# Optimization experiments

Measured on AMD Instinct MI355X. Metric: run time of the kernel, lower is better.

Reference implementation:

```python
import jax, jax.numpy as jnp
import numpy as np

NEG_INF = -1e10


def setup_inputs() -> dict:
    key = jax.random.key(0)
    ks = jax.random.split(key, 9)
    B, S, H, E = 64, 4096, 512, 512
    hidden = jax.random.normal(ks[0], (B, H), dtype=jnp.float32)
    encoder_outputs = jax.random.normal(ks[1], (B, S, E), dtype=jnp.float32)
    mask = jax.random.randint(ks[2], (B, S), 0, 2, dtype=jnp.int32)
    s = 1.0 / np.sqrt(H)
    Wq = jax.random.uniform(ks[3], (H, H), jnp.float32, -s, s)
    bq = jax.random.uniform(ks[4], (H,), jnp.float32, -s, s)
    se = 1.0 / np.sqrt(E)
    Wk = jax.random.uniform(ks[5], (E, H), jnp.float32, -se, se)
    bk = jax.random.uniform(ks[6], (H,), jnp.float32, -se, se)
    Wv = jax.random.uniform(ks[7], (H, 1), jnp.float32, -s, s)
    bv = jax.random.uniform(ks[8], (1,), jnp.float32, -s, s)
    return {"hidden": hidden, "encoder_outputs": encoder_outputs, "mask": mask,
            "Wq": Wq, "bq": bq, "Wk": Wk, "bk": bk, "Wv": Wv, "bv": bv}


def reference(hidden, encoder_outputs, mask, Wq, bq, Wk, bk, Wv, bv):
    # query projection: (B, H) -> broadcast over src_len
    q = hidden @ Wq + bq                       # (B, H)
    k = jnp.einsum('bse,eh->bsh', encoder_outputs, Wk) + bk  # (B, S, H)
    energy = jnp.tanh(q[:, None, :] + k)       # (B, S, H)
    scores = jnp.einsum('bsh,h->bs', energy, Wv[:, 0]) + bv[0]  # (B, S)
    scores = jnp.where(mask == 0, NEG_INF, scores)
    attn = jax.nn.softmax(scores, axis=1)      # (B, S)
    context = jnp.einsum('bs,bse->be', attn, encoder_outputs)   # (B, E)
    return context, attn
```

## Files before the change

### kernel.cpp

```cpp
#include <hip/hip_runtime.h>
#include <hip/hip_bf16.h>

#define B_ 64
#define S_ 4096
#define H_ 512
#define E_ 512
#define NEG_INF_ -1e10f

typedef __attribute__((ext_vector_type(8))) short short8;
typedef __attribute__((ext_vector_type(16))) float f32x16;

static __device__ __forceinline__ unsigned short f2bf(float f) {
    union { float f; unsigned u; } v; v.f = f;
    unsigned x = v.u;
    x += 0x7FFFu + ((x >> 16) & 1u);
    return (unsigned short)(x >> 16);
}

static __device__ __forceinline__ unsigned pk2(float lo, float hi) {
    float2 f; f.x = lo; f.y = hi;
    union { __hip_bfloat162 h; unsigned u; } c;
    c.h = __float22bfloat162_rn(f);
    return c.u;
}

static __device__ __forceinline__ void gload_lds16(const void* g, void* l) {
    __builtin_amdgcn_global_load_lds(
        (const __attribute__((address_space(1))) void*)g,
        (__attribute__((address_space(3))) void*)l, 16, 0, 0);
}

#define VMCNT6 do { asm volatile("s_waitcnt vmcnt(6)" ::: "memory"); __builtin_amdgcn_sched_barrier(0); } while (0)
#define VMCNT0 do { asm volatile("s_waitcnt vmcnt(0)" ::: "memory"); __builtin_amdgcn_sched_barrier(0); } while (0)
#define LGKM0  do { asm volatile("s_waitcnt lgkmcnt(0)" ::: "memory"); __builtin_amdgcn_sched_barrier(0); } while (0)

__global__ void prep_wkt(const float* __restrict__ wk, unsigned short* __restrict__ wkt) {
    int idx = blockIdx.x * 256 + threadIdx.x;
    int h = idx >> 9, e = idx & 511;
    wkt[idx] = f2bf(wk[e * H_ + h]);
}

__global__ void prep_qb(const float* __restrict__ hidden, const float* __restrict__ wq,
                        const float* __restrict__ bq, const float* __restrict__ bk,
                        float* __restrict__ qb) {
    __shared__ float hid[H_];
    int b = blockIdx.x, t = threadIdx.x;
    hid[t]       = hidden[b * H_ + t];
    hid[t + 256] = hidden[b * H_ + t + 256];
    __syncthreads();
    for (int hh = t; hh < H_; hh += 256) {
        float s = 0.f;
        for (int e = 0; e < H_; ++e) s += hid[e] * wq[e * H_ + hh];
        qb[b * H_ + hh] = s + bq[hh] + bk[hh];
    }
}

__global__ __launch_bounds__(256, 4) void scores_kernel(
    const float* __restrict__ enc, const unsigned short* __restrict__ wkt,
    const float* __restrict__ qb, const float* __restrict__ wv,
    float* __restrict__ part)
{
    __shared__ char lds[40960];

    int id = blockIdx.x;
    int xcd = id & 7, qq = id >> 3;
    int logical = xcd * 1024 + qq;
    int b  = logical >> 7;
    int r  = logical & 127;
    int st = r >> 2, nt = r & 3;
    int s0 = st * 128;

    const int tid  = threadIdx.x;
    const int lane = tid & 63;
    const int wave = tid >> 6;
    const int wr   = wave >> 1;
    const int wc   = wave & 1;
    const int l31  = lane & 31;
    const int g    = lane >> 5;

    const float* encb = enc + ((size_t)b * S_ + s0) * E_;

    const int arow   = tid & 127;
    const int aksl0  = (tid >> 7) * 2;
    const float* aptr = encb + (size_t)arow * 512 + aksl0 * 8;
    const int asrow  = arow & 31;
    const int aslb   = (arow >> 5) * 4 + aksl0;
    char* const awb0 = (char*)0 + asrow * 256 + (((aslb + 0 + asrow) & 15) << 4);
    char* const awb1 = (char*)0 + asrow * 256 + (((aslb + 1 + asrow) & 15) << 4);

    auto loadA = [&](int kc, float4 (&st_)[4]) {
        const float* p = aptr + kc * 32;
        st_[0] = *(const float4*)(p);
        st_[1] = *(const float4*)(p + 4);
        st_[2] = *(const float4*)(p + 8);
        st_[3] = *(const float4*)(p + 12);
    };
    auto writeA = [&](char* buf, const float4 (&st_)[4]) {
        union { short8 s; unsigned u[4]; } u0, u1;
        u0.u[0] = pk2(st_[0].x, st_[0].y); u0.u[1] = pk2(st_[0].z, st_[0].w);
        u0.u[2] = pk2(st_[1].x, st_[1].y); u0.u[3] = pk2(st_[1].z, st_[1].w);
        u1.u[0] = pk2(st_[2].x, st_[2].y); u1.u[1] = pk2(st_[2].z, st_[2].w);
        u1.u[2] = pk2(st_[3].x, st_[3].y); u1.u[3] = pk2(st_[3].z, st_[3].w);
        *(short8*)(buf + (size_t)awb0) = u0.s;
        *(short8*)(buf + (size_t)awb1) = u1.s;
    };
    auto stageB = [&](int kc, char* buf) {
#pragma unroll
        for (int p = 0; p < 2; ++p) {
            int gi0 = p * 256 + wave * 64;
            char* db = buf + gi0 * 16;
            int gi = gi0 + lane;
            int sn = gi >> 4, ss = gi & 15;
            int sl = ss ^ (sn & 15);
            int n  = (sl >> 2) * 32 + sn;
            const unsigned short* gp = wkt + (size_t)(nt * 128 + n) * 512 + kc * 32 + (sl & 3) * 8;
            gload_lds16(gp, db);
        }
    };

    f32x16 acc[2][2];
#pragma unroll
    for (int mr = 0; mr < 2; ++mr)
#pragma unroll
        for (int nf = 0; nf < 2; ++nf)
#pragma unroll
            for (int e = 0; e < 16; ++e) acc[mr][nf][e] = 0.f;

    float4 ra[4], rb[4];

    stageB(0, lds + 16384);          loadA(0, ra);
    stageB(1, lds + 16384 + 8192);   loadA(1, rb);

#pragma unroll
    for (int kc = 0; kc < 16; ++kc) {
        if (kc < 15) { VMCNT6; } else { VMCNT0; }
        char* Ab = lds + (kc & 1) * 8192;
        if (kc & 1) writeA(Ab, rb); else writeA(Ab, ra);
        LGKM0;
        __builtin_amdgcn_s_barrier();
        __builtin_amdgcn_sched_barrier(0);
        if (kc < 14) {
            stageB(kc + 2, lds + 16384 + ((kc + 2) % 3) * 8192);
            if (kc & 1) loadA(kc + 2, rb); else loadA(kc + 2, ra);
        }
        const char* Bb = lds + 16384 + (kc % 3) * 8192;
        __builtin_amdgcn_s_setprio(1);
#pragma unroll
        for (int ks = 0; ks < 2; ++ks) {
            short8 af[2], bf[2];
#pragma unroll
            for (int mr = 0; mr < 2; ++mr) {
                int sl = (wr * 2 + mr) * 4 + ks * 2 + g;
                af[mr] = *(const short8*)(Ab + l31 * 256 + (((sl + l31) & 15) << 4));
            }
#pragma unroll
            for (int nf = 0; nf < 2; ++nf) {
                int sl = (wc * 2 + nf) * 4 + ks * 2 + g;
                bf[nf] = *(const short8*)(Bb + l31 * 256 + ((sl ^ (l31 & 15)) << 4));
            }
            acc[0][0] = __builtin_amdgcn_mfma_f32_32x32x16_bf16(af[0], bf[0], acc[0][0], 0, 0, 0);
            acc[0][1] = __builtin_amdgcn_mfma_f32_32x32x16_bf16(af[0], bf[1], acc[0][1], 0, 0, 0);
            acc[1][0] = __builtin_amdgcn_mfma_f32_32x32x16_bf16(af[1], bf[0], acc[1][0], 0, 0, 0);
            acc[1][1] = __builtin_amdgcn_mfma_f32_32x32x16_bf16(af[1], bf[1], acc[1][1], 0, 0, 0);
        }
        __builtin_amdgcn_s_setprio(0);
    }

    float p[2][16];
#pragma unroll
    for (int nf = 0; nf < 2; ++nf) {
        int col = nt * 128 + wc * 64 + nf * 32 + l31;
        float qv  = qb[b * H_ + col];
        float wvv = wv[col];
#pragma unroll
        for (int mr = 0; mr < 2; ++mr)
#pragma unroll
            for (int e = 0; e < 16; ++e) {
                float x  = qv + acc[mr][nf][e];
                float ex = __expf(2.f * x);
                float th = 1.f - 2.f / (ex + 1.f);
                float v  = wvv * th;
                p[mr][e] = nf ? (p[mr][e] + v) : v;
            }
    }

    __syncthreads();
    float* ps = (float*)lds;
#pragma unroll
    for (int mr = 0; mr < 2; ++mr)
#pragma unroll
        for (int e = 0; e < 16; ++e) {
            int row = mr * 32 + (e & 3) + 8 * (e >> 2) + 4 * g;
            ps[(wave * 64 + row) * 36 + l31] = p[mr][e];
        }
    __syncthreads();
    float rsum = 0.f;
    {
        const float* myrow = ps + (size_t)(wave * 64 + lane) * 36;
#pragma unroll
        for (int j = 0; j < 8; ++j) {
            float4 v = *(const float4*)(myrow + j * 4);
            rsum += (v.x + v.y) + (v.z + v.w);
        }
    }
    float* pf = (float*)(lds + 36864);
    pf[wave * 64 + lane] = rsum;
    __syncthreads();
    if (tid < 128) {
        int wr2 = tid >> 6, rr = tid & 63;
        float v = pf[(wr2 * 2 + 0) * 64 + rr] + pf[(wr2 * 2 + 1) * 64 + rr];
        int s = s0 + wr2 * 64 + rr;
        part[((size_t)b * S_ + s) * 4 + nt] = v;
    }
}

__global__ void softmax_kernel(const float* __restrict__ part, const int* __restrict__ mask,
                               const float* __restrict__ bvp, float* __restrict__ attn) {
    __shared__ float red[8];
    int b = blockIdx.x, tid = threadIdx.x;
    int wid = tid >> 6, lane = tid & 63;
    float bv0 = bvp[0];
    float vals[8];
    float mx = -3.4e38f;
#pragma unroll
    for (int i = 0; i < 8; ++i) {
        int s = i * 512 + tid;
        float4 v = *(const float4*)(part + ((size_t)b * S_ + s) * 4);
        float sc = (v.x + v.y) + (v.z + v.w) + bv0;
        sc = mask[(size_t)b * S_ + s] ? sc : NEG_INF_;
        vals[i] = sc;
        mx = fmaxf(mx, sc);
    }
#pragma unroll
    for (int off = 1; off < 64; off <<= 1) mx = fmaxf(mx, __shfl_xor(mx, off));
    if (lane == 0) red[wid] = mx;
    __syncthreads();
    mx = red[0];
#pragma unroll
    for (int w = 1; w < 8; ++w) mx = fmaxf(mx, red[w]);
    __syncthreads();
    float sum = 0.f;
#pragma unroll
    for (int i = 0; i < 8; ++i) { vals[i] = __expf(vals[i] - mx); sum += vals[i]; }
#pragma unroll
    for (int off = 1; off < 64; off <<= 1) sum += __shfl_xor(sum, off);
    if (lane == 0) red[wid] = sum;
    __syncthreads();
    sum = red[0] + red[1] + red[2] + red[3] + red[4] + red[5] + red[6] + red[7];
    float inv = 1.f / sum;
#pragma unroll
    for (int i = 0; i < 8; ++i) attn[(size_t)b * S_ + i * 512 + tid] = vals[i] * inv;
}

__global__ void ctx_partial(const float* __restrict__ attn, const float* __restrict__ enc,
                            float* __restrict__ part) {
    __shared__ float a[256];
    int c = blockIdx.x, b = blockIdx.y, t = threadIdx.x;
    a[t] = attn[(size_t)b * S_ + c * 256 + t];
    __syncthreads();
    const float* ep = enc + (size_t)b * S_ * E_ + (size_t)c * 256 * E_ + t * 2;
    float x = 0.f, y = 0.f;
#pragma unroll 4
    for (int s = 0; s < 256; ++s) {
        float2 v = *(const float2*)(ep + (size_t)s * E_);
        x += a[s] * v.x;
        y += a[s] * v.y;
    }
    float* o = part + ((size_t)c * B_ + b) * E_ + t * 2;
    o[0] = x; o[1] = y;
}

__global__ void ctx_reduce(const float* __restrict__ part, float* __restrict__ ctx) {
    int idx = blockIdx.x * 256 + threadIdx.x;
    float s = 0.f;
#pragma unroll
    for (int c = 0; c < 16; ++c) s += part[(size_t)c * (B_ * E_) + idx];
    ctx[idx] = s;
}

extern "C" void kernel_launch(void* const* d_in, const int* in_sizes, int n_in,
                              void* d_out, int out_size, void* d_ws, size_t ws_size,
                              hipStream_t stream) {
    const float* hidden = (const float*)d_in[0];
    const float* enc    = (const float*)d_in[1];
    const int*   mask   = (const int*)d_in[2];
    const float* Wq     = (const float*)d_in[3];
    const float* bq     = (const float*)d_in[4];
    const float* Wk     = (const float*)d_in[5];
    const float* bk     = (const float*)d_in[6];
    const float* Wv     = (const float*)d_in[7];
    const float* bv     = (const float*)d_in[8];

    float* out  = (float*)d_out;
    char*  ws   = (char*)d_ws;
    float*          qbuf   = (float*)ws;
    unsigned short* wkt    = (unsigned short*)(ws + 131072);
    float*          pscore = (float*)(ws + 655360);
    float*          cpart  = (float*)(ws + 655360);

    float* ctx  = out;
    float* attn = out + B_ * E_;

    prep_wkt<<<1024, 256, 0, stream>>>(Wk, wkt);
    prep_qb<<<64, 256, 0, stream>>>(hidden, Wq, bq, bk, qbuf);
    scores_kernel<<<8192, 256, 0, stream>>>(enc, wkt, qbuf, Wv, pscore);
    softmax_kernel<<<64, 512, 0, stream>>>(pscore, mask, bv, attn);
    ctx_partial<<<dim3(16, 64), 256, 0, stream>>>(attn, enc, cpart);
    ctx_reduce<<<128, 256, 0, stream>>>(cpart, ctx);
}
```

Before: 506.5 us.

## Coalesce encoder A-tile loads across threads and relax occupancy hint

Remaps the fp32 encoder tile loads so that 8 consecutive threads read one contiguous 128-byte row segment, replacing the old pattern where each thread read 64 contiguous bytes from a different row. The LDS writes become 8-byte swizzled stores that keep the existing read layout. It also lowers the launch-bounds occupancy hint from 4 to 3 blocks per CU and removes the setprio wrapping around the MFMA section. The goal is better global-memory coalescing on the memory-bound encoder stream, at the cost of more and smaller LDS stores and possibly lower occupancy.

```diff
diff --git a/kernel.cpp b/kernel.cpp
--- a/kernel.cpp
+++ b/kernel.cpp
@@ -55,7 +55,7 @@
     }
 }
 
-__global__ __launch_bounds__(256, 4) void scores_kernel(
+__global__ __launch_bounds__(256, 3) void scores_kernel(
     const float* __restrict__ enc, const unsigned short* __restrict__ wkt,
     const float* __restrict__ qb, const float* __restrict__ wv,
     float* __restrict__ part)
@@ -80,29 +80,24 @@
 
     const float* encb = enc + ((size_t)b * S_ + s0) * E_;
 
-    const int arow   = tid & 127;
-    const int aksl0  = (tid >> 7) * 2;
-    const float* aptr = encb + (size_t)arow * 512 + aksl0 * 8;
-    const int asrow  = arow & 31;
-    const int aslb   = (arow >> 5) * 4 + aksl0;
-    char* const awb0 = (char*)0 + asrow * 256 + (((aslb + 0 + asrow) & 15) << 4);
-    char* const awb1 = (char*)0 + asrow * 256 + (((aslb + 1 + asrow) & 15) << 4);
+    const int srow = tid >> 3;
+    const int fl   = tid & 7;
+    const float* aptr = encb + (size_t)srow * 512 + fl * 4;
 
     auto loadA = [&](int kc, float4 (&st_)[4]) {
-        const float* p = aptr + kc * 32;
-        st_[0] = *(const float4*)(p);
-        st_[1] = *(const float4*)(p + 4);
-        st_[2] = *(const float4*)(p + 8);
-        st_[3] = *(const float4*)(p + 12);
+#pragma unroll
+        for (int j = 0; j < 4; ++j)
+            st_[j] = *(const float4*)(aptr + j * 16384 + kc * 32);
     };
     auto writeA = [&](char* buf, const float4 (&st_)[4]) {
-        union { short8 s; unsigned u[4]; } u0, u1;
-        u0.u[0] = pk2(st_[0].x, st_[0].y); u0.u[1] = pk2(st_[0].z, st_[0].w);
-        u0.u[2] = pk2(st_[1].x, st_[1].y); u0.u[3] = pk2(st_[1].z, st_[1].w);
-        u1.u[0] = pk2(st_[2].x, st_[2].y); u1.u[1] = pk2(st_[2].z, st_[2].w);
-        u1.u[2] = pk2(st_[3].x, st_[3].y); u1.u[3] = pk2(st_[3].z, st_[3].w);
-        *(short8*)(buf + (size_t)awb0) = u0.s;
-        *(short8*)(buf + (size_t)awb1) = u1.s;
+#pragma unroll
+        for (int j = 0; j < 4; ++j) {
+            int sst = ((j * 4 + (fl >> 1)) + srow) & 15;
+            uint2 w;
+            w.x = pk2(st_[j].x, st_[j].y);
+            w.y = pk2(st_[j].z, st_[j].w);
+            *(uint2*)(buf + srow * 256 + sst * 16 + (fl & 1) * 8) = w;
+        }
     };
     auto stageB = [&](int kc, char* buf) {
 #pragma unroll
@@ -144,7 +139,6 @@
             if (kc & 1) loadA(kc + 2, rb); else loadA(kc + 2, ra);
         }
         const char* Bb = lds + 16384 + (kc % 3) * 8192;
-        __builtin_amdgcn_s_setprio(1);
 #pragma unroll
         for (int ks = 0; ks < 2; ++ks) {
             short8 af[2], bf[2];
@@ -163,7 +157,6 @@
             acc[1][0] = __builtin_amdgcn_mfma_f32_32x32x16_bf16(af[1], bf[0], acc[1][0], 0, 0, 0);
             acc[1][1] = __builtin_amdgcn_mfma_f32_32x32x16_bf16(af[1], bf[1], acc[1][1], 0, 0, 0);
         }
-        __builtin_amdgcn_s_setprio(0);
     }
 
     float p[2][16];
```

Measured after the change: 498.0 us. Within noise of the previous version (-1.7%).
